# Kernel tuning notes

Measured on AMD Instinct MI355X. Metric: run time of the kernel, lower is better.

## Reference

```python
import jax, jax.numpy as jnp
import numpy as np

D_MODEL = 1024
N_HEADS = 16
D_K = D_MODEL // N_HEADS
MAX_REL = 128
SCALE = 1.0 / np.sqrt(D_K)
TEMP = 1.0


def setup_inputs() -> dict:
    key = jax.random.key(0)
    ks = jax.random.split(key, 12)
    B, S = 4, 1024
    inp = {
        "query": jax.random.normal(ks[0], (B, S, D_MODEL), jnp.float32),
        "key": jax.random.normal(ks[1], (B, S, D_MODEL), jnp.float32),
        "value": jax.random.normal(ks[2], (B, S, D_MODEL), jnp.float32),
        "mask": jnp.ones((B, S), jnp.int32),
        "w_q": jax.random.normal(ks[3], (D_MODEL, D_MODEL), jnp.float32) * 0.03,
        "b_q": jnp.zeros((D_MODEL,), jnp.float32),
        "w_k": jax.random.normal(ks[4], (D_MODEL, D_MODEL), jnp.float32) * 0.03,
        "b_k": jnp.zeros((D_MODEL,), jnp.float32),
        "w_v": jax.random.normal(ks[5], (D_MODEL, D_MODEL), jnp.float32) * 0.03,
        "b_v": jnp.zeros((D_MODEL,), jnp.float32),
        "w_o": jax.random.normal(ks[6], (D_MODEL, D_MODEL), jnp.float32) * 0.03,
        "b_o": jnp.zeros((D_MODEL,), jnp.float32),
        "rel_k": jax.random.normal(ks[7], (2 * MAX_REL + 1, D_K), jnp.float32),
        "rel_v": jax.random.normal(ks[8], (2 * MAX_REL + 1, D_K), jnp.float32),
    }
    return inp


def _relative_positions(seq_len):
    pos = jnp.arange(seq_len)
    rel = pos[None, :] - pos[:, None]  # [S, S]
    return jnp.clip(rel, -MAX_REL, MAX_REL) + MAX_REL


def reference(query, key, value, mask, w_q, b_q, w_k, b_k, w_v, b_v, w_o, b_o, rel_k, rel_v):
    B, S, _ = query.shape
    # projections (torch Linear: x @ W.T + b)
    Q = (query @ w_q.T + b_q).reshape(B, S, N_HEADS, D_K).transpose(0, 2, 1, 3)  # [B,H,S,d]
    K = (key @ w_k.T + b_k).reshape(B, S, N_HEADS, D_K).transpose(0, 2, 1, 3)
    V = (value @ w_v.T + b_v).reshape(B, S, N_HEADS, D_K).transpose(0, 2, 1, 3)

    scores = jnp.einsum("bhld,bhrd->bhlr", Q, K) * SCALE  # [B,H,S,S]

    rel_idx = _relative_positions(S)                      # [S,S] int
    rpk = rel_k[rel_idx]                                  # [S,S,d]
    scores = scores + jnp.einsum("bhld,lrd->bhlr", Q, rpk)

    scores = scores / TEMP
    m = mask[:, None, None, :]                            # [B,1,1,S]
    scores = jnp.where(m == 0, -1e9, scores)

    attn = jax.nn.softmax(scores, axis=-1)                # [B,H,S,S]
    context = jnp.einsum("bhlr,bhrd->bhld", attn, V)
    rpv = rel_v[rel_idx]                                  # [S,S,d]
    context = context + jnp.einsum("bhlr,lrd->bhld", attn, rpv)

    context = context.transpose(0, 2, 1, 3).reshape(B, S, D_MODEL)
    out = context @ w_o.T + b_o
    return out
```

## Files before the change

kernel.cpp:

```cpp
#include <hip/hip_runtime.h>
#include <hip/hip_bf16.h>

#define S_LEN  1024
#define DMODEL 1024
#define NHEADS 16
#define DK     64
#define SCALE  0.125f

typedef __bf16 bf16x8_t __attribute__((ext_vector_type(8)));
typedef __bf16 bf16x4_t __attribute__((ext_vector_type(4)));
typedef float  f32x4_t  __attribute__((ext_vector_type(4)));

#define MFMA16(A, B, C) __builtin_amdgcn_mfma_f32_16x16x32_bf16((A), (B), (C), 0, 0, 0)

__device__ __forceinline__ void async16(const void* g, void* l) {
    __builtin_amdgcn_global_load_lds(
        (const __attribute__((address_space(1))) unsigned int*)g,
        (__attribute__((address_space(3))) unsigned int*)l, 16, 0, 0);
}

__global__ __launch_bounds__(256) void cast_all_kernel(
    const float* __restrict__ q, const float* __restrict__ k, const float* __restrict__ v,
    const float* __restrict__ wq, const float* __restrict__ wk,
    const float* __restrict__ wv, const float* __restrict__ wo,
    const float* __restrict__ relk, const float* __restrict__ relv,
    __bf16* __restrict__ Xbf, __bf16* __restrict__ Wall,
    __bf16* __restrict__ relkp, __bf16* __restrict__ rvT,
    __bf16* __restrict__ Wqlo)
{
    const long i = (long)blockIdx.x * 256 + threadIdx.x;
    if (i < 3145728) {
        const int z   = (int)(i >> 20);
        const long rem = i & 1048575;
        const float4 s = ((const float4*)(z == 0 ? q : (z == 1 ? k : v)))[rem];
        bf16x4_t h;
        h[0] = (__bf16)s.x; h[1] = (__bf16)s.y; h[2] = (__bf16)s.z; h[3] = (__bf16)s.w;
        *(bf16x4_t*)(Xbf + ((size_t)z << 22) + rem * 4) = h;
    } else if (i < 3145728 + 1048576) {
        const long wi = i - 3145728;
        const int z   = (int)(wi >> 18);
        const long rem = wi & 262143;
        const float* src = (z == 0) ? wq : (z == 1) ? wk : (z == 2) ? wv : wo;
        const float4 s = ((const float4*)src)[rem];
        const float xs[4] = {s.x, s.y, s.z, s.w};
        bf16x4_t h;
        #pragma unroll
        for (int t = 0; t < 4; ++t) h[t] = (__bf16)xs[t];
        *(bf16x4_t*)(Wall + ((size_t)z << 20) + rem * 4) = h;
        if (z == 0) {
            bf16x4_t l;
            #pragma unroll
            for (int t = 0; t < 4; ++t) l[t] = (__bf16)(xs[t] - (float)h[t]);
            *(bf16x4_t*)(Wqlo + rem * 4) = l;
        }
    } else if (i < 3145728 + 1048576 + 4352) {
        const long ri = i - (3145728 + 1048576);
        const int j  = (int)(ri >> 4);
        const int d4 = (int)(ri & 15) * 4;
        bf16x4_t h, l;
        if (j < 257) {
            const float4 s = *(const float4*)(relk + j * 64 + d4);
            const float xs[4] = {s.x, s.y, s.z, s.w};
            #pragma unroll
            for (int t = 0; t < 4; ++t) {
                h[t] = (__bf16)xs[t];
                l[t] = (__bf16)(xs[t] - (float)h[t]);
            }
        } else {
            #pragma unroll
            for (int t = 0; t < 4; ++t) { h[t] = (__bf16)0.f; l[t] = (__bf16)0.f; }
        }
        *(bf16x4_t*)(relkp + j * 64 + d4) = h;
        *(bf16x4_t*)(relkp + 17408 + j * 64 + d4) = l;
    } else if (i < 3145728 + 1048576 + 4352 + 4608) {
        const long ri = i - (3145728 + 1048576 + 4352);
        const int d  = (int)(ri / 72);
        const int j4 = (int)(ri % 72) * 4;
        bf16x4_t o;
        #pragma unroll
        for (int t = 0; t < 4; ++t) {
            const int j = j4 + t;
            o[t] = (j < 257) ? (__bf16)relv[j * 64 + d] : (__bf16)0.f;
        }
        *(bf16x4_t*)(rvT + d * 288 + j4) = o;
    }
}

__device__ __forceinline__ void gemm128_core(
    const __bf16* __restrict__ A, const __bf16* __restrict__ W,
    __bf16* As, __bf16* Ws, f32x4_t acc[4][4])
{
    const int tid  = threadIdx.x;
    const int lane = tid & 63;
    const int quad = lane >> 4;
    const int l15  = lane & 15;
    const int wid  = tid >> 6;
    const int wm = wid >> 1, wn = wid & 1;

    for (int kt = 0; kt < 32; ++kt) {
        #pragma unroll
        for (int r = 0; r < 2; ++r) {
            const int c = r * 256 + tid;
            const int row = c >> 2, kb = c & 3;
            async16(A + row * 1024 + kt * 32 + kb * 8, As + c * 8);
            async16(W + row * 1024 + kt * 32 + kb * 8, Ws + c * 8);
        }
        __syncthreads();
        bf16x8_t af[4], wf[4];
        #pragma unroll
        for (int i = 0; i < 4; ++i) {
            af[i] = *(const bf16x8_t*)(As + (wm * 64 + i * 16 + l15) * 32 + quad * 8);
            wf[i] = *(const bf16x8_t*)(Ws + (wn * 64 + i * 16 + l15) * 32 + quad * 8);
        }
        #pragma unroll
        for (int i = 0; i < 4; ++i)
            #pragma unroll
            for (int j = 0; j < 4; ++j)
                acc[i][j] = MFMA16(af[i], wf[j], acc[i][j]);
        __syncthreads();
    }
}

__global__ __launch_bounds__(256) void gemm_qkv_kernel(
    const __bf16* __restrict__ Xbf, const __bf16* __restrict__ Wall,
    const __bf16* __restrict__ Wqlo,
    const float* __restrict__ bq, const float* __restrict__ bk, const float* __restrict__ bv,
    __bf16* __restrict__ QKVh)
{
    __shared__ __bf16 As[4096], Ws[4096];
    const int z = blockIdx.z;
    const __bf16* A = Xbf + (size_t)z * 4194304 + (size_t)blockIdx.y * 131072;
    const __bf16* W = Wall + (size_t)z * 1048576 + (size_t)blockIdx.x * 131072;
    f32x4_t acc[4][4];
    #pragma unroll
    for (int i = 0; i < 4; ++i)
        #pragma unroll
        for (int j = 0; j < 4; ++j)
            acc[i][j] = (f32x4_t){0.f, 0.f, 0.f, 0.f};

    gemm128_core(A, W, As, Ws, acc);
    if (z == 0)
        gemm128_core(A, Wqlo + (size_t)blockIdx.x * 131072, As, Ws, acc);

    const int tid = threadIdx.x, lane = tid & 63, quad = lane >> 4, l15 = lane & 15;
    const int wid = tid >> 6, wm = wid >> 1, wn = wid & 1;
    const int m0 = blockIdx.y * 128 + wm * 64;
    const int n0 = blockIdx.x * 128 + wn * 64;
    const float* bias = (z == 0) ? bq : ((z == 1) ? bk : bv);
    __bf16* dst = QKVh + (size_t)z * 4194304;

    if (z < 2) {
        #pragma unroll
        for (int j = 0; j < 4; ++j) {
            const int n = n0 + j * 16 + l15;
            const float bn = bias[n];
            #pragma unroll
            for (int i = 0; i < 4; ++i) {
                #pragma unroll
                for (int v = 0; v < 4; ++v) {
                    const int m = m0 + i * 16 + quad * 4 + v;
                    dst[((((m >> 10) * 16 + (n >> 6)) << 16)) + ((m & 1023) << 6) + (n & 63)]
                        = (__bf16)(acc[i][j][v] + bn);
                }
            }
        }
    } else {
        #pragma unroll
        for (int j = 0; j < 4; ++j) {
            const int n = n0 + j * 16 + l15;
            const float bn = bias[n];
            #pragma unroll
            for (int i = 0; i < 4; ++i) {
                const int m = m0 + i * 16 + quad * 4;
                bf16x4_t pk;
                #pragma unroll
                for (int v = 0; v < 4; ++v) pk[v] = (__bf16)(acc[i][j][v] + bn);
                const int s = m & 1023, d = n & 63;
                const size_t idx = (((size_t)((m >> 10) * 16 + (n >> 6))) << 16)
                                 + (size_t)(s >> 5) * 2048 + d * 32 + (s & 31);
                *(bf16x4_t*)(dst + idx) = pk;
            }
        }
    }
}

__global__ __launch_bounds__(256) void gemm_out_kernel(
    const __bf16* __restrict__ ctx, const __bf16* __restrict__ Wo,
    const float* __restrict__ bo, float* __restrict__ out)
{
    __shared__ __bf16 As[4096], Ws[4096];
    const __bf16* A = ctx + (size_t)blockIdx.y * 131072;
    const __bf16* W = Wo + (size_t)blockIdx.x * 131072;
    f32x4_t acc[4][4];
    #pragma unroll
    for (int i = 0; i < 4; ++i)
        #pragma unroll
        for (int j = 0; j < 4; ++j)
            acc[i][j] = (f32x4_t){0.f, 0.f, 0.f, 0.f};
    gemm128_core(A, W, As, Ws, acc);

    const int tid = threadIdx.x, lane = tid & 63, quad = lane >> 4, l15 = lane & 15;
    const int wid = tid >> 6, wm = wid >> 1, wn = wid & 1;
    const int m0 = blockIdx.y * 128 + wm * 64;
    const int n0 = blockIdx.x * 128 + wn * 64;
    #pragma unroll
    for (int j = 0; j < 4; ++j) {
        const int n = n0 + j * 16 + l15;
        const float bn = bo[n];
        #pragma unroll
        for (int i = 0; i < 4; ++i)
            #pragma unroll
            for (int v = 0; v < 4; ++v) {
                const int m = m0 + i * 16 + quad * 4 + v;
                out[(size_t)m * 1024 + n] = acc[i][j][v] + bn;
            }
    }
}

__global__ __launch_bounds__(256, 4) void attn_far_kernel(
    const __bf16* __restrict__ Qh, const __bf16* __restrict__ Kh,
    const __bf16* __restrict__ Vt, const __bf16* __restrict__ relkp,
    const int* __restrict__ mask, const float* __restrict__ relv,
    float* __restrict__ OfarG, float* __restrict__ rsG)
{
    __shared__ __align__(16) __bf16 Ks[2048];
    __shared__ __align__(16) __bf16 Vs[2048];
    __shared__ __align__(16) __bf16 p_s[4][16][40];

    const int tid = threadIdx.x, lane = tid & 63, wid = tid >> 6;
    const int quad = lane >> 4, l15 = lane & 15;
    const int lin = blockIdx.x;
    const int slot = lin >> 3;
    const int bh = (lin & 7) + 8 * (slot >> 4);
    const int chunk = slot & 15;
    const int b = bh >> 4;
    const int t0w = chunk * 4 + wid;
    const int l0 = t0w * 16;

    const __bf16* Qbase = Qh + (size_t)bh * 65536;
    const __bf16* Kbase = Kh + (size_t)bh * 65536;
    const __bf16* Vbase = Vt + (size_t)bh * 65536;
    const int* maskb = mask + b * 1024;

    const bf16x8_t aq0 = *(const bf16x8_t*)(Qbase + (l0 + l15) * 64 + quad * 8);
    const bf16x8_t aq1 = *(const bf16x8_t*)(Qbase + (l0 + l15) * 64 + 32 + quad * 8);

    float c0[4], c1[4];
    {
        const int jr = (l15 == 1) ? 256 : 0;
        const bf16x8_t bh0 = *(const bf16x8_t*)(relkp + jr * 64 + quad * 8);
        const bf16x8_t bh1 = *(const bf16x8_t*)(relkp + jr * 64 + 32 + quad * 8);
        const bf16x8_t bl0 = *(const bf16x8_t*)(relkp + 17408 + jr * 64 + quad * 8);
        const bf16x8_t bl1 = *(const bf16x8_t*)(relkp + 17408 + jr * 64 + 32 + quad * 8);
        f32x4_t cr = (f32x4_t){0.f, 0.f, 0.f, 0.f};
        cr = MFMA16(aq0, bl0, cr);
        cr = MFMA16(aq1, bl1, cr);
        cr = MFMA16(aq0, bh0, cr);
        cr = MFMA16(aq1, bh1, cr);
        #pragma unroll
        for (int v = 0; v < 4; ++v) {
            c0[v] = __shfl(cr[v], (lane & 48), 64);
            c1[v] = __shfl(cr[v], (lane & 48) | 1, 64);
        }
    }

    int gK[2], lK[2], gV[2], lV[2];
    #pragma unroll
    for (int ii = 0; ii < 2; ++ii) {
        const int ch = (wid & 1) * 128 + ii * 64 + lane;
        {
            const int r = ch >> 3, p = ch & 7, g = p ^ (r & 7);
            gK[ii] = r * 64 + g * 8;
            lK[ii] = ch * 8;
        }
        {
            const int d = ch >> 2, p = ch & 3, g = p ^ ((d >> 1) & 3);
            gV[ii] = d * 32 + g * 8;
            lV[ii] = ch * 8;
        }
    }

    f32x4_t o[4];
    #pragma unroll
    for (int dt = 0; dt < 4; ++dt) o[dt] = (f32x4_t){0.f, 0.f, 0.f, 0.f};
    float e0[4] = {0.f, 0.f, 0.f, 0.f};
    float e1[4] = {0.f, 0.f, 0.f, 0.f};

    for (int pc = 0; pc < 32; ++pc) {
        const int rb0 = pc * 32;
        if (wid < 2) {
            #pragma unroll
            for (int ii = 0; ii < 2; ++ii)
                async16(Kbase + rb0 * 64 + gK[ii], Ks + lK[ii]);
        } else {
            #pragma unroll
            for (int ii = 0; ii < 2; ++ii)
                async16(Vbase + pc * 2048 + gV[ii], Vs + lV[ii]);
        }
        __syncthreads();

        const int tI0 = pc * 2;
        const bool far0 = (tI0 <= t0w - 9) || (tI0 >= t0w + 9);
        const bool far1 = (tI0 + 1 <= t0w - 9) || (tI0 + 1 >= t0w + 9);
        if (far0 || far1) {
            #pragma unroll
            for (int sl = 0; sl < 2; ++sl) {
                const bool isFar = sl ? far1 : far0;
                if (isFar) {
                    const int R = sl * 16 + l15;
                    const bf16x8_t kb0 =
                        *(const bf16x8_t*)(Ks + R * 64 + (quad ^ (R & 7)) * 8);
                    const bf16x8_t kb1 =
                        *(const bf16x8_t*)(Ks + R * 64 + (((quad + 4) ^ (R & 7))) * 8);
                    f32x4_t s = (f32x4_t){0.f, 0.f, 0.f, 0.f};
                    s = MFMA16(aq0, kb0, s);
                    s = MFMA16(aq1, kb1, s);
                    const float madd = (maskb[rb0 + R] == 0) ? -1.0e9f : 0.f;
                    const bool isLo = (tI0 + sl < t0w);
                    #pragma unroll
                    for (int v = 0; v < 4; ++v) {
                        const float cc = isLo ? c0[v] : c1[v];
                        const float p = __expf(fmaf(s[v], SCALE, cc) + madd);
                        const __bf16 pb = (__bf16)p;
                        const float pf = (float)pb;
                        if (isLo) e0[v] += pf; else e1[v] += pf;
                        p_s[wid][quad * 4 + v][sl * 16 + l15] = pb;
                    }
                } else {
                    #pragma unroll
                    for (int v = 0; v < 4; ++v)
                        p_s[wid][quad * 4 + v][sl * 16 + l15] = (__bf16)0.f;
                }
            }
            const bf16x8_t pa = *(const bf16x8_t*)(&p_s[wid][l15][quad * 8]);
            #pragma unroll
            for (int dt = 0; dt < 4; ++dt) {
                const int D = dt * 16 + l15;
                const bf16x8_t vb =
                    *(const bf16x8_t*)(Vs + D * 32 + ((quad ^ ((D >> 1) & 3))) * 8);
                o[dt] = MFMA16(pa, vb, o[dt]);
            }
        }
        __syncthreads();
    }

    #pragma unroll
    for (int v = 0; v < 4; ++v)
        #pragma unroll
        for (int mm = 1; mm < 16; mm <<= 1) {
            e0[v] += __shfl_xor(e0[v], mm, 64);
            e1[v] += __shfl_xor(e1[v], mm, 64);
        }

    float* Od = OfarG + ((size_t)bh * 1024 + l0) * 64;
    #pragma unroll
    for (int dt = 0; dt < 4; ++dt) {
        const int d = dt * 16 + l15;
        const float rv0   = relv[d];
        const float rv256 = relv[256 * 64 + d];
        #pragma unroll
        for (int v = 0; v < 4; ++v)
            Od[(quad * 4 + v) * 64 + d] = o[dt][v] + e0[v] * rv0 + e1[v] * rv256;
    }
    if (l15 == 0) {
        #pragma unroll
        for (int v = 0; v < 4; ++v)
            rsG[bh * 1024 + l0 + quad * 4 + v] = e0[v] + e1[v];
    }
}

__global__ __launch_bounds__(64, 2) void attn_band_kernel(
    const __bf16* __restrict__ Qh, const __bf16* __restrict__ Kh,
    const __bf16* __restrict__ Vt, const __bf16* __restrict__ relkp,
    const __bf16* __restrict__ rvT, const int* __restrict__ mask,
    const float* __restrict__ relv,
    const float* __restrict__ OfarG, const float* __restrict__ rsG,
    __bf16* __restrict__ ctx)
{
    __shared__ __align__(16) __bf16 w_s[16][272];
    __shared__ __align__(16) __bf16 p_s[16][40];
    __shared__ __align__(16) _Float16 qr_s[16][276];

    const int lane = threadIdx.x & 63;
    const int quad = lane >> 4, l15 = lane & 15;
    const int lin = blockIdx.x;
    const int slot = lin >> 3;
    const int bh = (lin & 7) + 8 * (slot >> 6);
    const int t0 = slot & 63, l0 = t0 * 16;
    const int b = bh >> 4;

    const __bf16* Qbase = Qh + (size_t)bh * 65536;
    const __bf16* Kbase = Kh + (size_t)bh * 65536;
    const __bf16* Vbase = Vt + (size_t)bh * 65536;
    const int* maskb = mask + b * 1024;

    {
        uint4* wz = (uint4*)&w_s[0][0];
        for (int t = lane; t < 544; t += 64) wz[t] = (uint4){0u, 0u, 0u, 0u};
    }

    const bf16x8_t aq0 = *(const bf16x8_t*)(Qbase + (l0 + l15) * 64 + quad * 8);
    const bf16x8_t aq1 = *(const bf16x8_t*)(Qbase + (l0 + l15) * 64 + 32 + quad * 8);

    {
        const __bf16* rhi = relkp;
        const __bf16* rlo = relkp + 17408;
        #pragma unroll 4
        for (int nt = 0; nt < 17; ++nt) {
            const int j = nt * 16 + l15;
            const bf16x8_t h0 = *(const bf16x8_t*)(rhi + j * 64 + quad * 8);
            const bf16x8_t h1 = *(const bf16x8_t*)(rhi + j * 64 + 32 + quad * 8);
            const bf16x8_t g0 = *(const bf16x8_t*)(rlo + j * 64 + quad * 8);
            const bf16x8_t g1 = *(const bf16x8_t*)(rlo + j * 64 + 32 + quad * 8);
            f32x4_t c = (f32x4_t){0.f, 0.f, 0.f, 0.f};
            c = MFMA16(aq0, g0, c);
            c = MFMA16(aq1, g1, c);
            c = MFMA16(aq0, h0, c);
            c = MFMA16(aq1, h1, c);
            #pragma unroll
            for (int v = 0; v < 4; ++v)
                qr_s[quad * 4 + v][j] = (_Float16)c[v];
        }
    }

    const int tstart = t0 > 8 ? t0 - 8 : 0;
    const int tend   = t0 < 55 ? t0 + 8 : 63;
    const int nb = tend - tstart + 1;

    f32x4_t o[4];
    #pragma unroll
    for (int dt = 0; dt < 4; ++dt) o[dt] = (f32x4_t){0.f, 0.f, 0.f, 0.f};
    float rowsum[4] = {0.f, 0.f, 0.f, 0.f};
    float e0[4] = {0.f, 0.f, 0.f, 0.f};
    float e1[4] = {0.f, 0.f, 0.f, 0.f};

    bf16x8_t kb[2][2], vb[4];
    int rbA = tstart * 16;
    int rbB = rbA + 16;
    int mA, mB;
    {
        #pragma unroll
        for (int sl = 0; sl < 2; ++sl) {
            const int r = (sl ? rbB : rbA) + l15;
            kb[sl][0] = *(const bf16x8_t*)(Kbase + r * 64 + quad * 8);
            kb[sl][1] = *(const bf16x8_t*)(Kbase + r * 64 + 32 + quad * 8);
        }
        const int rr = (quad < 2) ? (rbA + quad * 8) : (rbB + (quad - 2) * 8);
        #pragma unroll
        for (int dt = 0; dt < 4; ++dt)
            vb[dt] = *(const bf16x8_t*)(Vbase + (rr >> 5) * 2048
                                        + (dt * 16 + l15) * 32 + (rr & 31));
        mA = maskb[rbA + l15];
        mB = maskb[rbB + l15];
    }

    for (int m = 0; m < nb; m += 2) {
        const bool hasB = (m + 1 < nb);
        const bool hasN = (m + 2 < nb);
        bf16x8_t kbn[2][2], vbn[4];
        int mAn = 0, mBn = 0, rbAn = 0, rbBn = 0;
        if (hasN) {
            rbAn = (tstart + m + 2) * 16;
            rbBn = (m + 3 < nb) ? rbAn + 16 : rbAn;
            #pragma unroll
            for (int sl = 0; sl < 2; ++sl) {
                const int r = (sl ? rbBn : rbAn) + l15;
                kbn[sl][0] = *(const bf16x8_t*)(Kbase + r * 64 + quad * 8);
                kbn[sl][1] = *(const bf16x8_t*)(Kbase + r * 64 + 32 + quad * 8);
            }
            const int rr = (quad < 2) ? (rbAn + quad * 8) : (rbBn + (quad - 2) * 8);
            #pragma unroll
            for (int dt = 0; dt < 4; ++dt)
                vbn[dt] = *(const bf16x8_t*)(Vbase + (rr >> 5) * 2048
                                             + (dt * 16 + l15) * 32 + (rr & 31));
            mAn = maskb[rbAn + l15];
            mBn = maskb[rbBn + l15];
        }

        #pragma unroll
        for (int slotn = 0; slotn < 2; ++slotn) {
            if (slotn == 1 && !hasB) {
                #pragma unroll
                for (int v = 0; v < 4; ++v)
                    p_s[quad * 4 + v][16 + l15] = (__bf16)0.f;
            } else {
                const int rb = slotn ? rbB : rbA;
                const int r = rb + l15;
                f32x4_t s = (f32x4_t){0.f, 0.f, 0.f, 0.f};
                s = MFMA16(aq0, kb[slotn][0], s);
                s = MFMA16(aq1, kb[slotn][1], s);
                const float madd = ((slotn ? mB : mA) == 0) ? -1.0e9f : 0.f;
                #pragma unroll
                for (int v = 0; v < 4; ++v) {
                    const int lrow = quad * 4 + v;
                    const int dd = r - (l0 + lrow);
                    int j = dd + 128; j = j < 0 ? 0 : (j > 256 ? 256 : j);
                    const float bias = (float)qr_s[lrow][j];
                    const float p = __expf(fmaf(s[v], SCALE, bias) + madd);
                    const __bf16 pb = (__bf16)p;
                    const float pf = (float)pb;
                    rowsum[v] += pf;
                    p_s[lrow][slotn * 16 + l15] = pb;
                    if (j == 0)        e0[v] += pf;
                    else if (j == 256) e1[v] += pf;
                    else               w_s[lrow][j] = pb;
                }
            }
        }
        const bf16x8_t pa = *(const bf16x8_t*)(&p_s[l15][quad * 8]);
        #pragma unroll
        for (int dt = 0; dt < 4; ++dt)
            o[dt] = MFMA16(pa, vb[dt], o[dt]);
        if (hasN) {
            #pragma unroll
            for (int sl = 0; sl < 2; ++sl) {
                kb[sl][0] = kbn[sl][0];
                kb[sl][1] = kbn[sl][1];
            }
            #pragma unroll
            for (int dt = 0; dt < 4; ++dt) vb[dt] = vbn[dt];
            mA = mAn; mB = mBn; rbA = rbAn; rbB = rbBn;
        }
    }

    #pragma unroll
    for (int v = 0; v < 4; ++v) {
        #pragma unroll
        for (int mm = 1; mm < 16; mm <<= 1) {
            rowsum[v] += __shfl_xor(rowsum[v], mm, 64);
            e0[v]     += __shfl_xor(e0[v], mm, 64);
            e1[v]     += __shfl_xor(e1[v], mm, 64);
        }
    }

    for (int kc = 0; kc < 8; ++kc) {
        const bf16x8_t wa = *(const bf16x8_t*)(&w_s[l15][kc * 32 + quad * 8]);
        #pragma unroll
        for (int dt = 0; dt < 4; ++dt) {
            const bf16x8_t rb =
                *(const bf16x8_t*)(rvT + (dt * 16 + l15) * 288 + kc * 32 + quad * 8);
            o[dt] = MFMA16(wa, rb, o[dt]);
        }
    }

    float rinv[4];
    #pragma unroll
    for (int v = 0; v < 4; ++v)
        rinv[v] = 1.f / (rowsum[v] + rsG[bh * 1024 + l0 + quad * 4 + v]);
    const float* Od = OfarG + ((size_t)bh * 1024 + l0) * 64;
    const int h = bh & 15;
    #pragma unroll
    for (int dt = 0; dt < 4; ++dt) {
        const int d = dt * 16 + l15;
        const float rv0   = relv[d];
        const float rv256 = relv[256 * 64 + d];
        #pragma unroll
        for (int v = 0; v < 4; ++v) {
            const int lrow = quad * 4 + v;
            const float val = (o[dt][v] + e0[v] * rv0 + e1[v] * rv256
                               + Od[lrow * 64 + d]) * rinv[v];
            ctx[((size_t)b * 1024 + l0 + lrow) * 1024 + h * 64 + d] = (__bf16)val;
        }
    }
}

extern "C" void kernel_launch(void* const* d_in, const int* in_sizes, int n_in,
                              void* d_out, int out_size, void* d_ws, size_t ws_size,
                              hipStream_t stream)
{
    const float* q    = (const float*)d_in[0];
    const float* k    = (const float*)d_in[1];
    const float* v    = (const float*)d_in[2];
    const int*   mask = (const int*)  d_in[3];
    const float* wq   = (const float*)d_in[4];
    const float* bq   = (const float*)d_in[5];
    const float* wk   = (const float*)d_in[6];
    const float* bk   = (const float*)d_in[7];
    const float* wv   = (const float*)d_in[8];
    const float* bv   = (const float*)d_in[9];
    const float* wo   = (const float*)d_in[10];
    const float* bo   = (const float*)d_in[11];
    const float* relk = (const float*)d_in[12];
    const float* relv = (const float*)d_in[13];

    __bf16* Xbf   = (__bf16*)d_ws;
    __bf16* Xgap  = Xbf   + 12582912;
    __bf16* Wqlo  = Xgap  + 4194304;
    __bf16* Wall  = Wqlo  + 1048576;
    __bf16* QKVh  = Wall  + 4194304;
    __bf16* ctx   = QKVh  + 12582912;
    __bf16* relkp = ctx   + 4194304;
    __bf16* rvT   = relkp + 34816;
    float*  OfarG = (float*)(rvT + 18432);
    float*  rsG   = OfarG + 4194304;

    cast_all_kernel<<<16419, 256, 0, stream>>>(q, k, v, wq, wk, wv, wo, relk, relv,
                                               Xbf, Wall, relkp, rvT, Wqlo);
    gemm_qkv_kernel<<<dim3(8, 32, 3), 256, 0, stream>>>(Xbf, Wall, Wqlo,
                                                        bq, bk, bv, QKVh);
    attn_far_kernel<<<1024, 256, 0, stream>>>(QKVh, QKVh + 4194304,
                                              QKVh + 2 * 4194304, relkp, mask,
                                              relv, OfarG, rsG);
    attn_band_kernel<<<4096, 64, 0, stream>>>(QKVh, QKVh + 4194304,
                                              QKVh + 2 * 4194304, relkp,
                                              rvT, mask, relv, OfarG, rsG, ctx);
    gemm_out_kernel<<<dim3(8, 32, 1), 256, 0, stream>>>(ctx, Wall + 3 * 1048576,
                                                        bo, (float*)d_out);
}
```

Baseline: 319.1 us.

## Split band attention across four waves per block with LDS merge

The band attention kernel now runs four waves per 16-row tile instead of one. Each wave handles a slice of the key blocks and of the relative-value chunks, then partial outputs, row sums and edge sums are reduced through shared memory. The rel-key bias table build is also shared across the waves. This shortens the serial per-wave loop and raises parallelism, at the cost of extra barriers, a shared-memory reduction, and dropping the explicit register prefetch of the next K/V blocks.

Result: no change. 321.0 us (+0.6%).

```diff
diff --git a/kernel.cpp b/kernel.cpp
--- a/kernel.cpp
+++ b/kernel.cpp
@@ -369,7 +369,7 @@
     }
 }
 
-__global__ __launch_bounds__(64, 2) void attn_band_kernel(
+__global__ __launch_bounds__(256, 4) void attn_band_kernel(
     const __bf16* __restrict__ Qh, const __bf16* __restrict__ Kh,
     const __bf16* __restrict__ Vt, const __bf16* __restrict__ relkp,
     const __bf16* __restrict__ rvT, const int* __restrict__ mask,
@@ -377,11 +377,15 @@
     const float* __restrict__ OfarG, const float* __restrict__ rsG,
     __bf16* __restrict__ ctx)
 {
+    __shared__ __align__(16) unsigned char u_raw[13056];
     __shared__ __align__(16) __bf16 w_s[16][272];
-    __shared__ __align__(16) __bf16 p_s[16][40];
-    __shared__ __align__(16) _Float16 qr_s[16][276];
-
-    const int lane = threadIdx.x & 63;
+    __shared__ __align__(16) __bf16 p_s[4][16][40];
+
+    _Float16 (*qr)[276] = (_Float16 (*)[276])u_raw;
+    float (*mrg)[16][68] = (float (*)[16][68])u_raw;
+
+    const int tid = threadIdx.x;
+    const int lane = tid & 63, wid = tid >> 6;
     const int quad = lane >> 4, l15 = lane & 15;
     const int lin = blockIdx.x;
     const int slot = lin >> 3;
@@ -396,7 +400,7 @@
 
     {
         uint4* wz = (uint4*)&w_s[0][0];
-        for (int t = lane; t < 544; t += 64) wz[t] = (uint4){0u, 0u, 0u, 0u};
+        for (int t = tid; t < 544; t += 256) wz[t] = (uint4){0u, 0u, 0u, 0u};
     }
 
     const bf16x8_t aq0 = *(const bf16x8_t*)(Qbase + (l0 + l15) * 64 + quad * 8);
@@ -405,8 +409,7 @@
     {
         const __bf16* rhi = relkp;
         const __bf16* rlo = relkp + 17408;
-        #pragma unroll 4
-        for (int nt = 0; nt < 17; ++nt) {
+        for (int nt = wid; nt < 17; nt += 4) {
             const int j = nt * 16 + l15;
             const bf16x8_t h0 = *(const bf16x8_t*)(rhi + j * 64 + quad * 8);
             const bf16x8_t h1 = *(const bf16x8_t*)(rhi + j * 64 + 32 + quad * 8);
@@ -419,13 +422,16 @@
             c = MFMA16(aq1, h1, c);
             #pragma unroll
             for (int v = 0; v < 4; ++v)
-                qr_s[quad * 4 + v][j] = (_Float16)c[v];
-        }
-    }
+                qr[quad * 4 + v][j] = (_Float16)c[v];
+        }
+    }
+    __syncthreads();
 
     const int tstart = t0 > 8 ? t0 - 8 : 0;
     const int tend   = t0 < 55 ? t0 + 8 : 63;
     const int nb = tend - tstart + 1;
+    const int sw = (nb * wid) >> 2;
+    const int ew = (nb * (wid + 1)) >> 2;
 
     f32x4_t o[4];
     #pragma unroll
@@ -434,92 +440,67 @@
     float e0[4] = {0.f, 0.f, 0.f, 0.f};
     float e1[4] = {0.f, 0.f, 0.f, 0.f};
 
-    bf16x8_t kb[2][2], vb[4];
-    int rbA = tstart * 16;
-    int rbB = rbA + 16;
-    int mA, mB;
-    {
-        #pragma unroll
-        for (int sl = 0; sl < 2; ++sl) {
-            const int r = (sl ? rbB : rbA) + l15;
-            kb[sl][0] = *(const bf16x8_t*)(Kbase + r * 64 + quad * 8);
-            kb[sl][1] = *(const bf16x8_t*)(Kbase + r * 64 + 32 + quad * 8);
-        }
+    for (int i = sw; i < ew; i += 2) {
+        const bool hasB = (i + 1 < ew);
+        const int rbA = (tstart + i) * 16;
+        const int rbB = hasB ? rbA + 16 : rbA;
+        const int rA = rbA + l15, rB = rbB + l15;
+        const bf16x8_t ka0 = *(const bf16x8_t*)(Kbase + rA * 64 + quad * 8);
+        const bf16x8_t ka1 = *(const bf16x8_t*)(Kbase + rA * 64 + 32 + quad * 8);
+        const bf16x8_t kb0 = *(const bf16x8_t*)(Kbase + rB * 64 + quad * 8);
+        const bf16x8_t kb1 = *(const bf16x8_t*)(Kbase + rB * 64 + 32 + quad * 8);
         const int rr = (quad < 2) ? (rbA + quad * 8) : (rbB + (quad - 2) * 8);
+        bf16x8_t vb[4];
         #pragma unroll
         for (int dt = 0; dt < 4; ++dt)
             vb[dt] = *(const bf16x8_t*)(Vbase + (rr >> 5) * 2048
                                         + (dt * 16 + l15) * 32 + (rr & 31));
-        mA = maskb[rbA + l15];
-        mB = maskb[rbB + l15];
-    }
-
-    for (int m = 0; m < nb; m += 2) {
-        const bool hasB = (m + 1 < nb);
-        const bool hasN = (m + 2 < nb);
-        bf16x8_t kbn[2][2], vbn[4];
-        int mAn = 0, mBn = 0, rbAn = 0, rbBn = 0;
-        if (hasN) {
-            rbAn = (tstart + m + 2) * 16;
-            rbBn = (m + 3 < nb) ? rbAn + 16 : rbAn;
-            #pragma unroll
-            for (int sl = 0; sl < 2; ++sl) {
-                const int r = (sl ? rbBn : rbAn) + l15;
-                kbn[sl][0] = *(const bf16x8_t*)(Kbase + r * 64 + quad * 8);
-                kbn[sl][1] = *(const bf16x8_t*)(Kbase + r * 64 + 32 + quad * 8);
-            }
-            const int rr = (quad < 2) ? (rbAn + quad * 8) : (rbBn + (quad - 2) * 8);
-            #pragma unroll
-            for (int dt = 0; dt < 4; ++dt)
-                vbn[dt] = *(const bf16x8_t*)(Vbase + (rr >> 5) * 2048
-                                             + (dt * 16 + l15) * 32 + (rr & 31));
-            mAn = maskb[rbAn + l15];
-            mBn = maskb[rbBn + l15];
-        }
+        const int mA = maskb[rA];
+        const int mB = maskb[rB];
 
         #pragma unroll
         for (int slotn = 0; slotn < 2; ++slotn) {
             if (slotn == 1 && !hasB) {
                 #pragma unroll
                 for (int v = 0; v < 4; ++v)
-                    p_s[quad * 4 + v][16 + l15] = (__bf16)0.f;
+                    p_s[wid][quad * 4 + v][16 + l15] = (__bf16)0.f;
             } else {
-                const int rb = slotn ? rbB : rbA;
-                const int r = rb + l15;
+                const int r = slotn ? rB : rA;
                 f32x4_t s = (f32x4_t){0.f, 0.f, 0.f, 0.f};
-                s = MFMA16(aq0, kb[slotn][0], s);
-                s = MFMA16(aq1, kb[slotn][1], s);
+                s = MFMA16(aq0, slotn ? kb0 : ka0, s);
+                s = MFMA16(aq1, slotn ? kb1 : ka1, s);
                 const float madd = ((slotn ? mB : mA) == 0) ? -1.0e9f : 0.f;
                 #pragma unroll
                 for (int v = 0; v < 4; ++v) {
                     const int lrow = quad * 4 + v;
                     const int dd = r - (l0 + lrow);
                     int j = dd + 128; j = j < 0 ? 0 : (j > 256 ? 256 : j);
-                    const float bias = (float)qr_s[lrow][j];
+                    const float bias = (float)qr[lrow][j];
                     const float p = __expf(fmaf(s[v], SCALE, bias) + madd);
                     const __bf16 pb = (__bf16)p;
                     const float pf = (float)pb;
                     rowsum[v] += pf;
-                    p_s[lrow][slotn * 16 + l15] = pb;
+                    p_s[wid][lrow][slotn * 16 + l15] = pb;
                     if (j == 0)        e0[v] += pf;
                     else if (j == 256) e1[v] += pf;
                     else               w_s[lrow][j] = pb;
                 }
             }
         }
-        const bf16x8_t pa = *(const bf16x8_t*)(&p_s[l15][quad * 8]);
+        const bf16x8_t pa = *(const bf16x8_t*)(&p_s[wid][l15][quad * 8]);
         #pragma unroll
         for (int dt = 0; dt < 4; ++dt)
             o[dt] = MFMA16(pa, vb[dt], o[dt]);
-        if (hasN) {
-            #pragma unroll
-            for (int sl = 0; sl < 2; ++sl) {
-                kb[sl][0] = kbn[sl][0];
-                kb[sl][1] = kbn[sl][1];
-            }
-            #pragma unroll
-            for (int dt = 0; dt < 4; ++dt) vb[dt] = vbn[dt];
-            mA = mAn; mB = mBn; rbA = rbAn; rbB = rbBn;
+    }
+    __syncthreads();
+
+    for (int kc = wid; kc < 8; kc += 4) {
+        const bf16x8_t wa = *(const bf16x8_t*)(&w_s[l15][kc * 32 + quad * 8]);
+        #pragma unroll
+        for (int dt = 0; dt < 4; ++dt) {
+            const bf16x8_t rb =
+                *(const bf16x8_t*)(rvT + (dt * 16 + l15) * 288 + kc * 32 + quad * 8);
+            o[dt] = MFMA16(wa, rb, o[dt]);
         }
     }
 
@@ -533,33 +514,56 @@
         }
     }
 
-    for (int kc = 0; kc < 8; ++kc) {
-        const bf16x8_t wa = *(const bf16x8_t*)(&w_s[l15][kc * 32 + quad * 8]);
+    if (wid > 0) {
+        #pragma unroll
+        for (int dt = 0; dt < 4; ++dt)
+            #pragma unroll
+            for (int v = 0; v < 4; ++v)
+                mrg[wid - 1][quad * 4 + v][dt * 16 + l15] = o[dt][v];
+        if (l15 == 0) {
+            #pragma unroll
+            for (int v = 0; v < 4; ++v) {
+                mrg[wid - 1][quad * 4 + v][64] = rowsum[v];
+                mrg[wid - 1][quad * 4 + v][65] = e0[v];
+                mrg[wid - 1][quad * 4 + v][66] = e1[v];
+            }
+        }
+    }
+    __syncthreads();
+
+    if (wid == 0) {
+        #pragma unroll
+        for (int w = 0; w < 3; ++w) {
+            #pragma unroll
+            for (int dt = 0; dt < 4; ++dt)
+                #pragma unroll
+                for (int v = 0; v < 4; ++v)
+                    o[dt][v] += mrg[w][quad * 4 + v][dt * 16 + l15];
+            #pragma unroll
+            for (int v = 0; v < 4; ++v) {
+                rowsum[v] += mrg[w][quad * 4 + v][64];
+                e0[v]     += mrg[w][quad * 4 + v][65];
+                e1[v]     += mrg[w][quad * 4 + v][66];
+            }
+        }
+        float rinv[4];
+        #pragma unroll
+        for (int v = 0; v < 4; ++v)
+            rinv[v] = 1.f / (rowsum[v] + rsG[bh * 1024 + l0 + quad * 4 + v]);
+        const float* Od = OfarG + ((size_t)bh * 1024 + l0) * 64;
+        const int h = bh & 15;
         #pragma unroll
         for (int dt = 0; dt < 4; ++dt) {
-            const bf16x8_t rb =
-                *(const bf16x8_t*)(rvT + (dt * 16 + l15) * 288 + kc * 32 + quad * 8);
-            o[dt] = MFMA16(wa, rb, o[dt]);
-        }
-    }
-
-    float rinv[4];
-    #pragma unroll
-    for (int v = 0; v < 4; ++v)
-        rinv[v] = 1.f / (rowsum[v] + rsG[bh * 1024 + l0 + quad * 4 + v]);
-    const float* Od = OfarG + ((size_t)bh * 1024 + l0) * 64;
-    const int h = bh & 15;
-    #pragma unroll
-    for (int dt = 0; dt < 4; ++dt) {
-        const int d = dt * 16 + l15;
-        const float rv0   = relv[d];
-        const float rv256 = relv[256 * 64 + d];
-        #pragma unroll
-        for (int v = 0; v < 4; ++v) {
-            const int lrow = quad * 4 + v;
-            const float val = (o[dt][v] + e0[v] * rv0 + e1[v] * rv256
-                               + Od[lrow * 64 + d]) * rinv[v];
-            ctx[((size_t)b * 1024 + l0 + lrow) * 1024 + h * 64 + d] = (__bf16)val;
+            const int d = dt * 16 + l15;
+            const float rv0   = relv[d];
+            const float rv256 = relv[256 * 64 + d];
+            #pragma unroll
+            for (int v = 0; v < 4; ++v) {
+                const int lrow = quad * 4 + v;
+                const float val = (o[dt][v] + e0[v] * rv0 + e1[v] * rv256
+                                   + Od[lrow * 64 + d]) * rinv[v];
+                ctx[((size_t)b * 1024 + l0 + lrow) * 1024 + h * 64 + d] = (__bf16)val;
+            }
         }
     }
 }
@@ -601,9 +605,9 @@
     attn_far_kernel<<<1024, 256, 0, stream>>>(QKVh, QKVh + 4194304,
                                               QKVh + 2 * 4194304, relkp, mask,
                                               relv, OfarG, rsG);
-    attn_band_kernel<<<4096, 64, 0, stream>>>(QKVh, QKVh + 4194304,
-                                              QKVh + 2 * 4194304, relkp,
-                                              rvT, mask, relv, OfarG, rsG, ctx);
+    attn_band_kernel<<<4096, 256, 0, stream>>>(QKVh, QKVh + 4194304,
+                                               QKVh + 2 * 4194304, relkp,
+                                               rvT, mask, relv, OfarG, rsG, ctx);
     gemm_out_kernel<<<dim3(8, 32, 1), 256, 0, stream>>>(ctx, Wall + 3 * 1048576,
                                                         bo, (float*)d_out);
 }
```
